# Kernel tuning notes

Measured on AMD Instinct MI355X. Metric: run time of the kernel, lower is better.

Reference implementation:

```python
import jax, jax.numpy as jnp
import numpy as np

L, B, T, S, H, E, V = 2, 128, 64, 80, 512, 512, 32000


def setup_inputs() -> dict:
    key = jax.random.key(0)
    ks = jax.random.split(key, 16)
    s = 1.0 / np.sqrt(H)
    inp = {
        "tokens": jax.random.randint(ks[0], (T, B), 0, V),
        "h0": jax.random.normal(ks[1], (L, B, H), jnp.float32),
        "c0": jax.random.normal(ks[2], (L, B, H), jnp.float32),
        "context": jax.random.normal(ks[3], (B, S, H), jnp.float32),
        "emb_table": jax.random.normal(ks[4], (V, E), jnp.float32) * 0.02,
        # layer 0: input size E+H (input feeding), layer 1: input size H
        "Wih0": jax.random.uniform(ks[5], (4 * H, E + H), jnp.float32, -s, s),
        "Whh0": jax.random.uniform(ks[6], (4 * H, H), jnp.float32, -s, s),
        "bih0": jax.random.uniform(ks[7], (4 * H,), jnp.float32, -s, s),
        "bhh0": jax.random.uniform(ks[8], (4 * H,), jnp.float32, -s, s),
        "Wih1": jax.random.uniform(ks[9], (4 * H, H), jnp.float32, -s, s),
        "Whh1": jax.random.uniform(ks[10], (4 * H, H), jnp.float32, -s, s),
        "bih1": jax.random.uniform(ks[11], (4 * H,), jnp.float32, -s, s),
        "bhh1": jax.random.uniform(ks[12], (4 * H,), jnp.float32, -s, s),
        "W_in": jax.random.uniform(ks[13], (H, H), jnp.float32, -s, s),
        "W_out": jax.random.uniform(ks[14], (H, 2 * H), jnp.float32, -s, s),
    }
    return inp


def _lstm_cell(x, h, c, Wih, Whh, bih, bhh):
    gates = x @ Wih.T + bih + h @ Whh.T + bhh  # [B, 4H]
    i, f, g, o = jnp.split(gates, 4, axis=-1)  # torch LSTMCell gate order
    i, f, o = jax.nn.sigmoid(i), jax.nn.sigmoid(f), jax.nn.sigmoid(o)
    g = jnp.tanh(g)
    c1 = f * c + i * g
    h1 = o * jnp.tanh(c1)
    return h1, c1


def reference(tokens, h0, c0, context, emb_table, Wih0, Whh0, bih0, bhh0,
              Wih1, Whh1, bih1, bhh1, W_in, W_out):
    emb = emb_table[tokens]  # [T, B, E]

    def step(carry, emb_t):
        h, c, out_prev = carry
        x = jnp.concatenate([emb_t, out_prev], axis=1)  # input feeding [B, E+H]
        h0_, c0_ = _lstm_cell(x, h[0], c[0], Wih0, Whh0, bih0, bhh0)
        h1_, c1_ = _lstm_cell(h0_, h[1], c[1], Wih1, Whh1, bih1, bhh1)
        rnn_out = h1_
        # GlobalAttention (Luong general)
        q = rnn_out @ W_in.T                                  # [B, H]
        attn = jax.nn.softmax(jnp.einsum('bsh,bh->bs', context, q), axis=-1)
        wctx = jnp.einsum('bs,bsh->bh', attn, context)        # [B, H]
        out = jnp.tanh(jnp.concatenate([wctx, rnn_out], axis=1) @ W_out.T)
        new_carry = (jnp.stack([h0_, h1_]), jnp.stack([c0_, c1_]), out)
        return new_carry, (out, attn)

    init_out = jnp.zeros((tokens.shape[1], H), emb.dtype)
    (hT, cT, _), (outputs, attns) = jax.lax.scan(step, (h0, c0, init_out), emb)
    return outputs, (hT, cT), attns
```

## Files before the change

kernel.cpp:

```cpp
#include <hip/hip_runtime.h>
#include <hip/hip_fp16.h>
#include <cmath>

typedef _Float16 f16;
typedef _Float16 f16x8 __attribute__((ext_vector_type(8)));
typedef float f32x4 __attribute__((ext_vector_type(4)));
typedef unsigned long long u64;

constexpr int B = 128, T = 64, S = 80, H = 512;
constexpr int BH = B * H;
constexpr int NWG = 512;

#define LB256 __launch_bounds__(256)
#define MFMA16(a, b, c) __builtin_amdgcn_mfma_f32_16x16x32_f16(a, b, c, 0, 0, 0)

__device__ __forceinline__ void astore4(void* p, unsigned v) {
    __hip_atomic_store((unsigned*)p, v, __ATOMIC_RELAXED, __HIP_MEMORY_SCOPE_AGENT);
}
__device__ __forceinline__ void astoref(float* p, float v) {
    __hip_atomic_store(p, v, __ATOMIC_RELAXED, __HIP_MEMORY_SCOPE_AGENT);
}
__device__ __forceinline__ void astore8(void* p, u64 v) {
    __hip_atomic_store((u64*)p, v, __ATOMIC_RELAXED, __HIP_MEMORY_SCOPE_AGENT);
}
__device__ __forceinline__ u64 aload8(const void* p) {
    return __hip_atomic_load((const u64*)p, __ATOMIC_RELAXED, __HIP_MEMORY_SCOPE_AGENT);
}
__device__ __forceinline__ unsigned aload4(const void* p) {
    return __hip_atomic_load((const unsigned*)p, __ATOMIC_RELAXED, __HIP_MEMORY_SCOPE_AGENT);
}

__device__ __forceinline__ void dbar(unsigned* slots, unsigned* go,
                                     unsigned e, int wg) {
    __syncthreads();
    if (threadIdx.x == 0) astore4(&slots[wg * 4], e);
    if (wg == NWG - 1) {
        const int i0 = threadIdx.x * 2;
        while (aload4(&slots[i0 * 4]) < e) __builtin_amdgcn_s_sleep(1);
        while (aload4(&slots[(i0 + 1) * 4]) < e) __builtin_amdgcn_s_sleep(1);
        __syncthreads();
        if (threadIdx.x < 16) astore4(&go[threadIdx.x * 16], e);
    }
    if (threadIdx.x == 0) {
        while (aload4(&go[(wg & 15) * 16]) < e) __builtin_amdgcn_s_sleep(1);
    }
    __syncthreads();
    asm volatile("" ::: "memory");
}

__global__ LB256 void prep_all(
    const float* __restrict__ Wih0, const float* __restrict__ Whh0,
    const float* __restrict__ Wih1, const float* __restrict__ Whh1,
    const float* __restrict__ Wout, const float* __restrict__ Win,
    const float* __restrict__ bih0, const float* __restrict__ bhh0,
    const float* __restrict__ bih1, const float* __restrict__ bhh1,
    const float* __restrict__ h0,
    f16* __restrict__ WB0a, f16* __restrict__ WB0x, f16* __restrict__ WB1p,
    f16* __restrict__ WoutRf, f16* __restrict__ WcatT,
    float* __restrict__ bsum0, float* __restrict__ bsum1,
    f16* __restrict__ h0q, f16* __restrict__ h1q, f16* __restrict__ xq,
    unsigned* __restrict__ slots, unsigned* __restrict__ go)
{
    int stride = gridDim.x * blockDim.x;
    int idx = blockIdx.x * blockDim.x + threadIdx.x;
    for (int i = idx; i < 2048 * 512; i += stride) {
        int rp = i >> 9, k = i & 511;
        int h = rp >> 2, g = rp & 3, src = g * 512 + h;
        WB0a[i] = (f16)Wih0[src * 1024 + k];
    }
    for (int i = idx; i < 2048 * 1024; i += stride) {
        int rp = i >> 10, k = i & 1023;
        int h = rp >> 2, g = rp & 3, src = g * 512 + h;
        float v = (k < 512) ? Wih0[src * 1024 + 512 + k] : Whh0[src * 512 + (k - 512)];
        WB0x[i] = (f16)v;
    }
    for (int i = idx; i < 2048 * 1024; i += stride) {
        int rp = i >> 10, k = i & 1023;
        int h = rp >> 2, g = rp & 3, src = g * 512 + h;
        float v = (k < 512) ? Wih1[src * 512 + k] : Whh1[src * 512 + (k - 512)];
        WB1p[i] = (f16)v;
    }
    for (int i = idx; i < 512 * 512; i += stride) {
        int n = i >> 9, k = i & 511;
        WoutRf[i] = (f16)Wout[n * 1024 + 512 + k];
    }
    for (int i = idx; i < 1024 * 512; i += stride) {
        int r = i >> 9, k = i & 511;
        float v = (r < 512) ? Win[k * 512 + r] : Wout[(r - 512) * 1024 + k];
        WcatT[i] = (f16)v;
    }
    for (int i = idx; i < 2048; i += stride) {
        bsum0[i] = bih0[i] + bhh0[i];
        bsum1[i] = bih1[i] + bhh1[i];
    }
    for (int i = idx; i < BH; i += stride) {
        h0q[i] = (f16)h0[i];
        h1q[i] = (f16)h0[BH + i];
        xq[i] = (f16)0.f;
    }
    for (int i = idx; i < 2048; i += stride) slots[i] = 0u;
    for (int i = idx; i < 256; i += stride) go[i] = 0u;
}

__global__ LB256 void prep_emb(const int* __restrict__ tokens,
                               const float* __restrict__ embtab,
                               f16* __restrict__ embf16)
{
    int stride = gridDim.x * blockDim.x;
    for (int i = blockIdx.x * blockDim.x + threadIdx.x; i < T * B * 512; i += stride) {
        int e = i & 511;
        int tb = i >> 9;
        int tok = tokens[tb];
        embf16[i] = (f16)embtab[(size_t)tok * 512 + e];
    }
}

__global__ LB256 void gemm_ctx(const float* __restrict__ A32,
                               const f16* __restrict__ Wf,
                               f16* __restrict__ Cf)
{
    const int lane = threadIdx.x & 63;
    const int wave = threadIdx.x >> 6;
    const int quad = lane >> 4;
    const int wb = wave >> 1, wn = wave & 1;
    const int m = blockIdx.y * 32 + wb * 16 + (lane & 15);
    const int n = blockIdx.x * 32 + wn * 16 + (lane & 15);

    f32x4 acc = {0.f, 0.f, 0.f, 0.f};
    const float* ar = A32 + (size_t)m * 512;
    const f16* wr = Wf + (size_t)n * 512;
    #pragma unroll 4
    for (int i = 0; i < 16; ++i) {
        int k = i * 32 + quad * 8;
        float4 u0 = *(const float4*)(ar + k);
        float4 u1 = *(const float4*)(ar + k + 4);
        f16x8 av = { (f16)u0.x, (f16)u0.y, (f16)u0.z, (f16)u0.w,
                     (f16)u1.x, (f16)u1.y, (f16)u1.z, (f16)u1.w };
        f16x8 wv = *(const f16x8*)(wr + k);
        acc = MFMA16(av, wv, acc);
    }
    const int col = blockIdx.x * 32 + wn * 16 + (lane & 15);
    #pragma unroll
    for (int r = 0; r < 4; ++r) {
        int row = blockIdx.y * 32 + wb * 16 + quad * 4 + r;
        Cf[(size_t)row * 1024 + col] = (f16)acc[r];
    }
}

__global__ __launch_bounds__(256, 2) void decoder_persist(
    const f16* __restrict__ embf16,
    const f16* __restrict__ WB0a,
    const f16* __restrict__ WB0x,
    const f16* __restrict__ WB1p,
    const f16* __restrict__ WoutRf,
    const f16* __restrict__ ctxWV,
    const float* __restrict__ bsum0, const float* __restrict__ bsum1,
    const float* __restrict__ c0in,
    f16* __restrict__ h0q,
    f16* __restrict__ h1q,
    f16* __restrict__ xq,
    float* __restrict__ scb,
    f16* __restrict__ out2b,
    unsigned* __restrict__ slots, unsigned* __restrict__ go,
    float* __restrict__ out_outputs, float* __restrict__ out_attn,
    float* __restrict__ out_hT, float* __restrict__ out_cT)
{
    const int wg = blockIdx.x, tid = threadIdx.x;
    const int lane = tid & 63, wv_ = tid >> 6, quad = lane >> 4, m16 = lane & 15;
    const int mslice = wg >> 7;
    const int nslice = wg & 127;
    const int b0 = mslice * 32;
    const int rowbase = nslice * 16;

    __shared__ f16 WLA[16 * 1024];
    __shared__ f16 WLB[16 * 1024];
    __shared__ float gbuf[4][32][16];
    __shared__ float scf[80], pp[80];
    __shared__ unsigned o2buf[128];
    __shared__ f16 obuf[256];

    for (int i = tid; i < 2048; i += 256) {
        int r = i >> 7, g = i & 127, gp = g ^ (r & 7);
        *(f16x8*)(WLA + (r * 128 + gp) * 8) =
            *(const f16x8*)(WB0x + ((size_t)(rowbase + r)) * 1024 + g * 8);
        *(f16x8*)(WLB + (r * 128 + gp) * 8) =
            *(const f16x8*)(WB1p + ((size_t)(rowbase + r)) * 1024 + g * 8);
    }
    const int cb_ = b0 + (tid & 31);
    const int jp = (tid >> 5) * 2;
    const int ch = nslice * 4 + jp;
    float c0r[2], c1r[2], bi0[2][4], bi1[2][4];
    if (tid < 64) {
        #pragma unroll
        for (int j = 0; j < 2; ++j) {
            c0r[j] = c0in[cb_ * 512 + ch + j];
            c1r[j] = c0in[BH + cb_ * 512 + ch + j];
            #pragma unroll
            for (int g = 0; g < 4; ++g) {
                bi0[j][g] = bsum0[g * 512 + ch + j];
                bi1[j][g] = bsum1[g * 512 + ch + j];
            }
        }
    }
    const int b_s = wg >> 2;
    const int soff = (wg & 3) * 20;
    const int m2 = wg >> 5, n2 = wg & 31;
    const int b2 = wg >> 1, nh = wg & 1;
    unsigned ep = 0;
    __syncthreads();

    for (int t = 0; t < T; ++t) {
        const f16* EMBt = embf16 + (size_t)t * BH;
        const f16* XPt  = xq  + (size_t)t * BH;
        const f16* H0t  = h0q + (size_t)t * BH;
        const f16* H1t  = h1q + (size_t)t * BH;
        f16* H0n = h0q + (size_t)(t + 1) * BH;
        f16* H1n = h1q + (size_t)(t + 1) * BH;
        f16* XPn = xq  + (size_t)(t + 1) * BH;

        {
            f32x4 ac0 = {0.f, 0.f, 0.f, 0.f}, ac1 = {0.f, 0.f, 0.f, 0.f};
            const int a0r = (b0 + m16) * 512 + quad * 8;
            const int a1r = (b0 + 16 + m16) * 512 + quad * 8;
            const f16* wga = WB0a + (size_t)(rowbase + m16) * 512 + quad * 8;
            const int gq = quad;
            if (wv_ == 0) {
                #pragma unroll
                for (int ks = 0; ks < 12; ++ks) {
                    int k = ks * 32;
                    f16x8 w = *(const f16x8*)(wga + k);
                    ac0 = MFMA16(*(const f16x8*)(EMBt + a0r + k), w, ac0);
                    ac1 = MFMA16(*(const f16x8*)(EMBt + a1r + k), w, ac1);
                }
            } else if (wv_ == 1) {
                #pragma unroll
                for (int ks = 0; ks < 4; ++ks) {
                    int k = 384 + ks * 32;
                    f16x8 w = *(const f16x8*)(wga + k);
                    ac0 = MFMA16(*(const f16x8*)(EMBt + a0r + k), w, ac0);
                    ac1 = MFMA16(*(const f16x8*)(EMBt + a1r + k), w, ac1);
                }
                #pragma unroll
                for (int ks = 0; ks < 8; ++ks) {
                    int k = ks * 32;
                    int gr = (k >> 3) + gq, gp = gr ^ (m16 & 7);
                    f16x8 w = *(const f16x8*)(WLA + (m16 * 128 + gp) * 8);
                    ac0 = MFMA16(*(const f16x8*)(XPt + a0r + k), w, ac0);
                    ac1 = MFMA16(*(const f16x8*)(XPt + a1r + k), w, ac1);
                }
            } else if (wv_ == 2) {
                #pragma unroll
                for (int ks = 0; ks < 8; ++ks) {
                    int k = 256 + ks * 32;
                    int gr = (k >> 3) + gq, gp = gr ^ (m16 & 7);
                    f16x8 w = *(const f16x8*)(WLA + (m16 * 128 + gp) * 8);
                    ac0 = MFMA16(*(const f16x8*)(XPt + a0r + k), w, ac0);
                    ac1 = MFMA16(*(const f16x8*)(XPt + a1r + k), w, ac1);
                }
                #pragma unroll
                for (int ks = 0; ks < 4; ++ks) {
                    int k = ks * 32;
                    int gr = 64 + (k >> 3) + gq, gp = gr ^ (m16 & 7);
                    f16x8 w = *(const f16x8*)(WLA + (m16 * 128 + gp) * 8);
                    ac0 = MFMA16(*(const f16x8*)(H0t + a0r + k), w, ac0);
                    ac1 = MFMA16(*(const f16x8*)(H0t + a1r + k), w, ac1);
                }
            } else {
                #pragma unroll
                for (int ks = 0; ks < 12; ++ks) {
                    int k = 128 + ks * 32;
                    int gr = 64 + (k >> 3) + gq, gp = gr ^ (m16 & 7);
                    f16x8 w = *(const f16x8*)(WLA + (m16 * 128 + gp) * 8);
                    ac0 = MFMA16(*(const f16x8*)(H0t + a0r + k), w, ac0);
                    ac1 = MFMA16(*(const f16x8*)(H0t + a1r + k), w, ac1);
                }
            }
            #pragma unroll
            for (int r = 0; r < 4; ++r) {
                gbuf[wv_][quad * 4 + r][m16] = ac0[r];
                gbuf[wv_][16 + quad * 4 + r][m16] = ac1[r];
            }
            __syncthreads();
            if (tid < 64) {
                const int bl = tid & 31;
                float hv[2];
                #pragma unroll
                for (int j = 0; j < 2; ++j) {
                    int nl = (jp + j) * 4;
                    float z[4];
                    #pragma unroll
                    for (int g = 0; g < 4; ++g)
                        z[g] = gbuf[0][bl][nl + g] + gbuf[1][bl][nl + g] +
                               gbuf[2][bl][nl + g] + gbuf[3][bl][nl + g] + bi0[j][g];
                    float ig = 1.f / (1.f + expf(-z[0]));
                    float fg = 1.f / (1.f + expf(-z[1]));
                    float gg = tanhf(z[2]);
                    float og = 1.f / (1.f + expf(-z[3]));
                    float c = fg * c0r[j] + ig * gg;
                    c0r[j] = c;
                    hv[j] = og * tanhf(c);
                }
                union { f16 f[2]; unsigned u; } pk;
                pk.f[0] = (f16)hv[0]; pk.f[1] = (f16)hv[1];
                astore4(H0n + cb_ * 512 + ch, pk.u);
                if (t == T - 1) {
                    out_hT[cb_ * 512 + ch] = hv[0];
                    out_hT[cb_ * 512 + ch + 1] = hv[1];
                    out_cT[cb_ * 512 + ch] = c0r[0];
                    out_cT[cb_ * 512 + ch + 1] = c0r[1];
                }
            }
        }
        dbar(slots, go, ++ep, wg);

        {
            f32x4 ac0 = {0.f, 0.f, 0.f, 0.f}, ac1 = {0.f, 0.f, 0.f, 0.f};
            const int a0r = (b0 + m16) * 512 + quad * 8;
            const int a1r = (b0 + 16 + m16) * 512 + quad * 8;
            const f16* Asrc = (wv_ < 2) ? H0n : H1t;
            const int k0 = (wv_ & 1) * 256;
            const int gbase = ((wv_ < 2) ? 0 : 64) + (k0 >> 3);
            #pragma unroll
            for (int ks = 0; ks < 8; ++ks) {
                int k = k0 + ks * 32;
                int gr = gbase + ks * 4 + quad, gp = gr ^ (m16 & 7);
                f16x8 w = *(const f16x8*)(WLB + (m16 * 128 + gp) * 8);
                ac0 = MFMA16(*(const f16x8*)(Asrc + a0r + k), w, ac0);
                ac1 = MFMA16(*(const f16x8*)(Asrc + a1r + k), w, ac1);
            }
            #pragma unroll
            for (int r = 0; r < 4; ++r) {
                gbuf[wv_][quad * 4 + r][m16] = ac0[r];
                gbuf[wv_][16 + quad * 4 + r][m16] = ac1[r];
            }
            __syncthreads();
            if (tid < 64) {
                const int bl = tid & 31;
                float hv[2];
                #pragma unroll
                for (int j = 0; j < 2; ++j) {
                    int nl = (jp + j) * 4;
                    float z[4];
                    #pragma unroll
                    for (int g = 0; g < 4; ++g)
                        z[g] = gbuf[0][bl][nl + g] + gbuf[1][bl][nl + g] +
                               gbuf[2][bl][nl + g] + gbuf[3][bl][nl + g] + bi1[j][g];
                    float ig = 1.f / (1.f + expf(-z[0]));
                    float fg = 1.f / (1.f + expf(-z[1]));
                    float gg = tanhf(z[2]);
                    float og = 1.f / (1.f + expf(-z[3]));
                    float c = fg * c1r[j] + ig * gg;
                    c1r[j] = c;
                    hv[j] = og * tanhf(c);
                }
                union { f16 f[2]; unsigned u; } pk;
                pk.f[0] = (f16)hv[0]; pk.f[1] = (f16)hv[1];
                astore4(H1n + cb_ * 512 + ch, pk.u);
                if (t == T - 1) {
                    out_hT[BH + cb_ * 512 + ch] = hv[0];
                    out_hT[BH + cb_ * 512 + ch + 1] = hv[1];
                    out_cT[BH + cb_ * 512 + ch] = c1r[0];
                    out_cT[BH + cb_ * 512 + ch + 1] = c1r[1];
                }
            }
        }
        dbar(slots, go, ++ep, wg);

        {
            const f16* hrow = H1n + b_s * 512;
            f16x8 hfrag = *(const f16x8*)(hrow + lane * 8);
            #pragma unroll
            for (int i = 0; i < 5; ++i) {
                int s = soff + wv_ * 5 + i;
                const f16* cr = ctxWV + ((size_t)(b_s * 80 + s)) * 1024 + lane * 8;
                f16x8 a = *(const f16x8*)cr;
                float d = 0.f;
                #pragma unroll
                for (int j = 0; j < 8; ++j) d += (float)a[j] * (float)hfrag[j];
                #pragma unroll
                for (int o = 32; o > 0; o >>= 1) d += __shfl_xor(d, o);
                if (lane == 0) astoref(&scb[b_s * 80 + s], d);
            }
            if (wg < 128) {
                f32x4 ac0 = {0.f, 0.f, 0.f, 0.f}, ac1 = {0.f, 0.f, 0.f, 0.f};
                const int bb0 = m2 * 32;
                const int a0r = (bb0 + m16) * 512 + quad * 8;
                const int a1r = (bb0 + 16 + m16) * 512 + quad * 8;
                const f16* wr = WoutRf + (size_t)(n2 * 16 + m16) * 512 + quad * 8;
                const int k0 = wv_ * 128;
                #pragma unroll
                for (int ks = 0; ks < 4; ++ks) {
                    int k = k0 + ks * 32;
                    f16x8 w = *(const f16x8*)(wr + k);
                    ac0 = MFMA16(*(const f16x8*)(H1n + a0r + k), w, ac0);
                    ac1 = MFMA16(*(const f16x8*)(H1n + a1r + k), w, ac1);
                }
                __syncthreads();
                #pragma unroll
                for (int r = 0; r < 4; ++r) {
                    gbuf[wv_][quad * 4 + r][m16] = ac0[r];
                    gbuf[wv_][16 + quad * 4 + r][m16] = ac1[r];
                }
                __syncthreads();
                const int bl = tid >> 3, np = (tid & 7) * 2;
                float v0 = gbuf[0][bl][np] + gbuf[1][bl][np] + gbuf[2][bl][np] + gbuf[3][bl][np];
                float v1 = gbuf[0][bl][np+1] + gbuf[1][bl][np+1] + gbuf[2][bl][np+1] + gbuf[3][bl][np+1];
                union { f16 f[2]; unsigned u; } pk;
                pk.f[0] = (f16)v0; pk.f[1] = (f16)v1;
                astore4(out2b + (bb0 + bl) * 512 + n2 * 16 + np, pk.u);
            }
        }
        dbar(slots, go, ++ep, wg);

        if (wg < 256) {
            if (wv_ == 0 && lane < 40) {
                union { u64 u; float f[2]; } v;
                v.u = aload8(&scb[b2 * 80 + lane * 2]);
                scf[lane * 2] = v.f[0];
                scf[lane * 2 + 1] = v.f[1];
            }
            if (tid < 128)
                o2buf[tid] = aload4((const unsigned*)(out2b + b2 * 512 + nh * 256) + tid);
            __syncthreads();
            if (wv_ == 0) {
                float e0 = scf[lane];
                float e1 = (lane < 16) ? scf[64 + lane] : -1e30f;
                float m = fmaxf(e0, e1);
                #pragma unroll
                for (int o = 32; o > 0; o >>= 1) m = fmaxf(m, __shfl_xor(m, o));
                float x0 = expf(e0 - m);
                float x1 = (lane < 16) ? expf(e1 - m) : 0.f;
                float su = x0 + x1;
                #pragma unroll
                for (int o = 32; o > 0; o >>= 1) su += __shfl_xor(su, o);
                float inv = 1.f / su;
                float p0 = x0 * inv;
                pp[lane] = p0;
                if (nh == 0) out_attn[((size_t)t * 128 + b2) * 80 + lane] = p0;
                if (lane < 16) {
                    float p1 = x1 * inv;
                    pp[64 + lane] = p1;
                    if (nh == 0) out_attn[((size_t)t * 128 + b2) * 80 + 64 + lane] = p1;
                }
            }
            __syncthreads();
            const int n = nh * 256 + tid;
            float acc = 0.f;
            const f16* cv = ctxWV + (size_t)b2 * 80 * 1024 + 512 + n;
            #pragma unroll 8
            for (int s = 0; s < 80; ++s) acc += pp[s] * (float)cv[(size_t)s * 1024];
            float o2 = (float)((const f16*)o2buf)[tid];
            float o = tanhf(acc + o2);
            out_outputs[(size_t)t * BH + b2 * 512 + n] = o;
            obuf[tid] = (f16)o;
            __syncthreads();
            if (tid < 64)
                astore8(XPn + b2 * 512 + nh * 256 + tid * 4, ((const u64*)obuf)[tid]);
        }
        dbar(slots, go, ++ep, wg);
    }
}

extern "C" void kernel_launch(void* const* d_in, const int* in_sizes, int n_in,
                              void* d_out, int out_size, void* d_ws, size_t ws_size,
                              hipStream_t stream)
{
    const int*   tokens  = (const int*)  d_in[0];
    const float* h0      = (const float*)d_in[1];
    const float* c0      = (const float*)d_in[2];
    const float* context = (const float*)d_in[3];
    const float* embtab  = (const float*)d_in[4];
    const float* Wih0    = (const float*)d_in[5];
    const float* Whh0    = (const float*)d_in[6];
    const float* bih0    = (const float*)d_in[7];
    const float* bhh0    = (const float*)d_in[8];
    const float* Wih1    = (const float*)d_in[9];
    const float* Whh1    = (const float*)d_in[10];
    const float* bih1    = (const float*)d_in[11];
    const float* bhh1    = (const float*)d_in[12];
    const float* Win     = (const float*)d_in[13];
    const float* Wout    = (const float*)d_in[14];

    float* outF        = (float*)d_out;
    float* out_outputs = outF;
    float* out_hT      = outF + (size_t)T * BH;
    float* out_cT      = out_hT + 2 * BH;
    float* out_attn    = out_cT + 2 * BH;

    char* w = (char*)d_ws;
    auto alloc = [&](size_t bytes) {
        char* p = w;
        w += (bytes + 255) & ~(size_t)255;
        return p;
    };
    f16*      WB0a   = (f16*)     alloc((size_t)2048 * 512 * 2);
    f16*      WB0x   = (f16*)     alloc((size_t)2048 * 1024 * 2);
    f16*      WB1p   = (f16*)     alloc((size_t)2048 * 1024 * 2);
    f16*      WoutRf = (f16*)     alloc((size_t)512 * 512 * 2);
    f16*      WcatT  = (f16*)     alloc((size_t)1024 * 512 * 2);
    f16*      embf16 = (f16*)     alloc((size_t)T * B * 512 * 2);
    f16*      ctxWV  = (f16*)     alloc((size_t)B * S * 1024 * 2);
    float*    bsum0  = (float*)   alloc(2048 * 4);
    float*    bsum1  = (float*)   alloc(2048 * 4);
    f16*      h0q    = (f16*)     alloc((size_t)(T + 1) * BH * 2);
    f16*      h1q    = (f16*)     alloc((size_t)(T + 1) * BH * 2);
    f16*      xq     = (f16*)     alloc((size_t)(T + 1) * BH * 2);
    float*    scb    = (float*)   alloc((size_t)B * 80 * 4);
    f16*      out2b  = (f16*)     alloc((size_t)B * 512 * 2);
    unsigned* slots  = (unsigned*)alloc(2048 * 4);
    unsigned* go     = (unsigned*)alloc(256 * 4);

    prep_all<<<1024, 256, 0, stream>>>(Wih0, Whh0, Wih1, Whh1, Wout, Win,
                                       bih0, bhh0, bih1, bhh1, h0,
                                       WB0a, WB0x, WB1p, WoutRf, WcatT,
                                       bsum0, bsum1, h0q, h1q, xq, slots, go);
    prep_emb<<<2048, 256, 0, stream>>>(tokens, embtab, embf16);
    gemm_ctx<<<dim3(32, 320), 256, 0, stream>>>(context, WcatT, ctxWV);

    decoder_persist<<<NWG, 256, 0, stream>>>(
        embf16, WB0a, WB0x, WB1p, WoutRf, ctxWV, bsum0, bsum1, c0,
        h0q, h1q, xq, scb, out2b, slots, go,
        out_outputs, out_attn, out_hT, out_cT);
}
```

Baseline: 2.078 ms.

## Replace grid-wide barriers with per-batch-slice barriers and fuse attention output stage

Swaps the global two-level barrier for a barrier that waits only on the 128 workgroups sharing the same batch slice. It also remaps workgroup indices so slices interleave. The attention score, softmax and output projection now run inside one phase per batch row. Each group computes its own scores and the Wout·h1 dot products redundantly, which removes one grid barrier and the scratch buffers per step. The cost is redundant score computation (4x per batch row) and scalar Wout dot products in place of MFMA.

```diff
diff --git a/kernel.cpp b/kernel.cpp
--- a/kernel.cpp
+++ b/kernel.cpp
@@ -17,32 +17,20 @@
 __device__ __forceinline__ void astore4(void* p, unsigned v) {
     __hip_atomic_store((unsigned*)p, v, __ATOMIC_RELAXED, __HIP_MEMORY_SCOPE_AGENT);
 }
-__device__ __forceinline__ void astoref(float* p, float v) {
-    __hip_atomic_store(p, v, __ATOMIC_RELAXED, __HIP_MEMORY_SCOPE_AGENT);
-}
 __device__ __forceinline__ void astore8(void* p, u64 v) {
     __hip_atomic_store((u64*)p, v, __ATOMIC_RELAXED, __HIP_MEMORY_SCOPE_AGENT);
 }
-__device__ __forceinline__ u64 aload8(const void* p) {
-    return __hip_atomic_load((const u64*)p, __ATOMIC_RELAXED, __HIP_MEMORY_SCOPE_AGENT);
-}
 __device__ __forceinline__ unsigned aload4(const void* p) {
     return __hip_atomic_load((const unsigned*)p, __ATOMIC_RELAXED, __HIP_MEMORY_SCOPE_AGENT);
 }
 
-__device__ __forceinline__ void dbar(unsigned* slots, unsigned* go,
-                                     unsigned e, int wg) {
+__device__ __forceinline__ void mbar(unsigned* slots, unsigned e,
+                                     int mslice, int nslice) {
     __syncthreads();
-    if (threadIdx.x == 0) astore4(&slots[wg * 4], e);
-    if (wg == NWG - 1) {
-        const int i0 = threadIdx.x * 2;
-        while (aload4(&slots[i0 * 4]) < e) __builtin_amdgcn_s_sleep(1);
-        while (aload4(&slots[(i0 + 1) * 4]) < e) __builtin_amdgcn_s_sleep(1);
-        __syncthreads();
-        if (threadIdx.x < 16) astore4(&go[threadIdx.x * 16], e);
-    }
-    if (threadIdx.x == 0) {
-        while (aload4(&go[(wg & 15) * 16]) < e) __builtin_amdgcn_s_sleep(1);
+    if (threadIdx.x == 0) astore4(&slots[(mslice * 128 + nslice) * 4], e);
+    if (threadIdx.x < 128) {
+        while (aload4(&slots[(mslice * 128 + threadIdx.x) * 4]) < e)
+            __builtin_amdgcn_s_sleep(1);
     }
     __syncthreads();
     asm volatile("" ::: "memory");
@@ -59,7 +47,7 @@
     f16* __restrict__ WoutRf, f16* __restrict__ WcatT,
     float* __restrict__ bsum0, float* __restrict__ bsum1,
     f16* __restrict__ h0q, f16* __restrict__ h1q, f16* __restrict__ xq,
-    unsigned* __restrict__ slots, unsigned* __restrict__ go)
+    unsigned* __restrict__ slots)
 {
     int stride = gridDim.x * blockDim.x;
     int idx = blockIdx.x * blockDim.x + threadIdx.x;
@@ -99,7 +87,6 @@
         xq[i] = (f16)0.f;
     }
     for (int i = idx; i < 2048; i += stride) slots[i] = 0u;
-    for (int i = idx; i < 256; i += stride) go[i] = 0u;
 }
 
 __global__ LB256 void prep_emb(const int* __restrict__ tokens,
@@ -159,16 +146,14 @@
     f16* __restrict__ h0q,
     f16* __restrict__ h1q,
     f16* __restrict__ xq,
-    float* __restrict__ scb,
-    f16* __restrict__ out2b,
-    unsigned* __restrict__ slots, unsigned* __restrict__ go,
+    unsigned* __restrict__ slots,
     float* __restrict__ out_outputs, float* __restrict__ out_attn,
     float* __restrict__ out_hT, float* __restrict__ out_cT)
 {
     const int wg = blockIdx.x, tid = threadIdx.x;
     const int lane = tid & 63, wv_ = tid >> 6, quad = lane >> 4, m16 = lane & 15;
-    const int mslice = wg >> 7;
-    const int nslice = wg & 127;
+    const int mslice = (wg & 7) >> 1;
+    const int nslice = ((wg >> 3) << 1) | (wg & 1);
     const int b0 = mslice * 32;
     const int rowbase = nslice * 16;
 
@@ -176,8 +161,9 @@
     __shared__ f16 WLB[16 * 1024];
     __shared__ float gbuf[4][32][16];
     __shared__ float scf[80], pp[80];
-    __shared__ unsigned o2buf[128];
-    __shared__ f16 obuf[256];
+    __shared__ float psum[2][128];
+    __shared__ __align__(8) f16 h1s[512];
+    __shared__ __align__(8) f16 obuf[128];
 
     for (int i = tid; i < 2048; i += 256) {
         int r = i >> 7, g = i & 127, gp = g ^ (r & 7);
@@ -202,10 +188,9 @@
             }
         }
     }
-    const int b_s = wg >> 2;
-    const int soff = (wg & 3) * 20;
-    const int m2 = wg >> 5, n2 = wg & 31;
-    const int b2 = wg >> 1, nh = wg & 1;
+    const int q = nslice & 3;
+    const int bloc = nslice >> 2;
+    const int cb2 = b0 + bloc;
     unsigned ep = 0;
     __syncthreads();
 
@@ -311,7 +296,7 @@
                 }
             }
         }
-        dbar(slots, go, ++ep, wg);
+        mbar(slots, ++ep, mslice, nslice);
 
         {
             f32x4 ac0 = {0.f, 0.f, 0.f, 0.f}, ac1 = {0.f, 0.f, 0.f, 0.f};
@@ -364,63 +349,25 @@
                 }
             }
         }
-        dbar(slots, go, ++ep, wg);
+        mbar(slots, ++ep, mslice, nslice);
 
         {
-            const f16* hrow = H1n + b_s * 512;
-            f16x8 hfrag = *(const f16x8*)(hrow + lane * 8);
-            #pragma unroll
-            for (int i = 0; i < 5; ++i) {
-                int s = soff + wv_ * 5 + i;
-                const f16* cr = ctxWV + ((size_t)(b_s * 80 + s)) * 1024 + lane * 8;
+            if (tid < 128)
+                ((u64*)h1s)[tid] = ((const u64*)(H1n + cb2 * 512))[tid];
+            __syncthreads();
+            f16x8 hfrag = *(const f16x8*)&h1s[lane * 8];
+            #pragma unroll 4
+            for (int i = 0; i < 20; ++i) {
+                int s = wv_ * 20 + i;
+                const f16* cr = ctxWV + ((size_t)(cb2 * 80 + s)) * 1024 + lane * 8;
                 f16x8 a = *(const f16x8*)cr;
                 float d = 0.f;
                 #pragma unroll
                 for (int j = 0; j < 8; ++j) d += (float)a[j] * (float)hfrag[j];
                 #pragma unroll
                 for (int o = 32; o > 0; o >>= 1) d += __shfl_xor(d, o);
-                if (lane == 0) astoref(&scb[b_s * 80 + s], d);
-            }
-            if (wg < 128) {
-                f32x4 ac0 = {0.f, 0.f, 0.f, 0.f}, ac1 = {0.f, 0.f, 0.f, 0.f};
-                const int bb0 = m2 * 32;
-                const int a0r = (bb0 + m16) * 512 + quad * 8;
-                const int a1r = (bb0 + 16 + m16) * 512 + quad * 8;
-                const f16* wr = WoutRf + (size_t)(n2 * 16 + m16) * 512 + quad * 8;
-                const int k0 = wv_ * 128;
-                #pragma unroll
-                for (int ks = 0; ks < 4; ++ks) {
-                    int k = k0 + ks * 32;
-                    f16x8 w = *(const f16x8*)(wr + k);
-                    ac0 = MFMA16(*(const f16x8*)(H1n + a0r + k), w, ac0);
-                    ac1 = MFMA16(*(const f16x8*)(H1n + a1r + k), w, ac1);
-                }
-                __syncthreads();
-                #pragma unroll
-                for (int r = 0; r < 4; ++r) {
-                    gbuf[wv_][quad * 4 + r][m16] = ac0[r];
-                    gbuf[wv_][16 + quad * 4 + r][m16] = ac1[r];
-                }
-                __syncthreads();
-                const int bl = tid >> 3, np = (tid & 7) * 2;
-                float v0 = gbuf[0][bl][np] + gbuf[1][bl][np] + gbuf[2][bl][np] + gbuf[3][bl][np];
-                float v1 = gbuf[0][bl][np+1] + gbuf[1][bl][np+1] + gbuf[2][bl][np+1] + gbuf[3][bl][np+1];
-                union { f16 f[2]; unsigned u; } pk;
-                pk.f[0] = (f16)v0; pk.f[1] = (f16)v1;
-                astore4(out2b + (bb0 + bl) * 512 + n2 * 16 + np, pk.u);
-            }
-        }
-        dbar(slots, go, ++ep, wg);
-
-        if (wg < 256) {
-            if (wv_ == 0 && lane < 40) {
-                union { u64 u; float f[2]; } v;
-                v.u = aload8(&scb[b2 * 80 + lane * 2]);
-                scf[lane * 2] = v.f[0];
-                scf[lane * 2 + 1] = v.f[1];
-            }
-            if (tid < 128)
-                o2buf[tid] = aload4((const unsigned*)(out2b + b2 * 512 + nh * 256) + tid);
+                if (lane == 0) scf[s] = d;
+            }
             __syncthreads();
             if (wv_ == 0) {
                 float e0 = scf[lane];
@@ -436,28 +383,51 @@
                 float inv = 1.f / su;
                 float p0 = x0 * inv;
                 pp[lane] = p0;
-                if (nh == 0) out_attn[((size_t)t * 128 + b2) * 80 + lane] = p0;
+                if (q == 0) out_attn[((size_t)t * 128 + cb2) * 80 + lane] = p0;
                 if (lane < 16) {
                     float p1 = x1 * inv;
                     pp[64 + lane] = p1;
-                    if (nh == 0) out_attn[((size_t)t * 128 + b2) * 80 + 64 + lane] = p1;
-                }
-            }
-            __syncthreads();
-            const int n = nh * 256 + tid;
+                    if (q == 0) out_attn[((size_t)t * 128 + cb2) * 80 + 64 + lane] = p1;
+                }
+            }
+            __syncthreads();
+            const int nl = tid & 127, kh = tid >> 7;
+            const int n = q * 128 + nl;
             float acc = 0.f;
-            const f16* cv = ctxWV + (size_t)b2 * 80 * 1024 + 512 + n;
-            #pragma unroll 8
-            for (int s = 0; s < 80; ++s) acc += pp[s] * (float)cv[(size_t)s * 1024];
-            float o2 = (float)((const f16*)o2buf)[tid];
-            float o = tanhf(acc + o2);
-            out_outputs[(size_t)t * BH + b2 * 512 + n] = o;
-            obuf[tid] = (f16)o;
-            __syncthreads();
-            if (tid < 64)
-                astore8(XPn + b2 * 512 + nh * 256 + tid * 4, ((const u64*)obuf)[tid]);
+            if (kh == 0) {
+                const f16* cv = ctxWV + (size_t)cb2 * 80 * 1024 + 512 + n;
+                #pragma unroll 8
+                for (int s = 0; s < 80; ++s) acc += pp[s] * (float)cv[(size_t)s * 1024];
+                const f16* wr = WoutRf + (size_t)n * 512;
+                #pragma unroll
+                for (int kk = 0; kk < 24; ++kk) {
+                    f16x8 w = *(const f16x8*)(wr + kk * 8);
+                    f16x8 h = *(const f16x8*)&h1s[kk * 8];
+                    #pragma unroll
+                    for (int j = 0; j < 8; ++j) acc += (float)w[j] * (float)h[j];
+                }
+            } else {
+                const f16* wr = WoutRf + (size_t)n * 512;
+                #pragma unroll
+                for (int kk = 24; kk < 64; ++kk) {
+                    f16x8 w = *(const f16x8*)(wr + kk * 8);
+                    f16x8 h = *(const f16x8*)&h1s[kk * 8];
+                    #pragma unroll
+                    for (int j = 0; j < 8; ++j) acc += (float)w[j] * (float)h[j];
+                }
+            }
+            psum[kh][nl] = acc;
+            __syncthreads();
+            if (tid < 128) {
+                float o = tanhf(psum[0][tid] + psum[1][tid]);
+                out_outputs[(size_t)t * BH + cb2 * 512 + n] = o;
+                obuf[tid] = (f16)o;
+            }
+            __syncthreads();
+            if (tid < 32)
+                astore8(XPn + cb2 * 512 + q * 128 + tid * 4, ((const u64*)obuf)[tid]);
         }
-        dbar(slots, go, ++ep, wg);
+        mbar(slots, ++ep, mslice, nslice);
     }
 }
 
@@ -505,20 +475,17 @@
     f16*      h0q    = (f16*)     alloc((size_t)(T + 1) * BH * 2);
     f16*      h1q    = (f16*)     alloc((size_t)(T + 1) * BH * 2);
     f16*      xq     = (f16*)     alloc((size_t)(T + 1) * BH * 2);
-    float*    scb    = (float*)   alloc((size_t)B * 80 * 4);
-    f16*      out2b  = (f16*)     alloc((size_t)B * 512 * 2);
     unsigned* slots  = (unsigned*)alloc(2048 * 4);
-    unsigned* go     = (unsigned*)alloc(256 * 4);
 
     prep_all<<<1024, 256, 0, stream>>>(Wih0, Whh0, Wih1, Whh1, Wout, Win,
                                        bih0, bhh0, bih1, bhh1, h0,
                                        WB0a, WB0x, WB1p, WoutRf, WcatT,
-                                       bsum0, bsum1, h0q, h1q, xq, slots, go);
+                                       bsum0, bsum1, h0q, h1q, xq, slots);
     prep_emb<<<2048, 256, 0, stream>>>(tokens, embtab, embf16);
     gemm_ctx<<<dim3(32, 320), 256, 0, stream>>>(context, WcatT, ctxWV);
 
     decoder_persist<<<NWG, 256, 0, stream>>>(
         embf16, WB0a, WB0x, WB1p, WoutRf, ctxWV, bsum0, bsum1, c0,
-        h0q, h1q, xq, scb, out2b, slots, go,
+        h0q, h1q, xq, slots,
         out_outputs, out_attn, out_hT, out_cT);
 }
```

New measurement: 3.165 ms. 1.52x slower.

## Remap workgroup-to-batch assignment so attention phases stay within an XCD

Applied to the files above, without the earlier changes.

Workgroup roles are re-indexed by wg&7 (likely the XCD id under round-robin dispatch), so each XCD owns a 16-batch slice for the score, W_out projection and softmax phases. The projection tile changes from 32 batch rows by 16 columns to 16 rows by 32 columns, sharing one A fragment across two MFMAs. The aim is to keep the data passed between phases within one XCD's L2 and to cut cross-die traffic, at the cost of relying on an assumed dispatch order and of changing which workgroups do the softmax work.

```diff
diff --git a/kernel.cpp b/kernel.cpp
--- a/kernel.cpp
+++ b/kernel.cpp
@@ -202,10 +202,12 @@
             }
         }
     }
-    const int b_s = wg >> 2;
-    const int soff = (wg & 3) * 20;
-    const int m2 = wg >> 5, n2 = wg & 31;
-    const int b2 = wg >> 1, nh = wg & 1;
+    const int xid = wg & 7;
+    const int xr = wg >> 3;
+    const int b_s = xid * 16 + (xr & 15);
+    const int soff = (xr >> 4) * 20;
+    const int b2 = xid * 16 + ((xr - 16) >> 1);
+    const int nh = (xr - 16) & 1;
     unsigned ep = 0;
     __syncthreads();
 
@@ -381,19 +383,18 @@
                 for (int o = 32; o > 0; o >>= 1) d += __shfl_xor(d, o);
                 if (lane == 0) astoref(&scb[b_s * 80 + s], d);
             }
-            if (wg < 128) {
+            if (xr < 16) {
                 f32x4 ac0 = {0.f, 0.f, 0.f, 0.f}, ac1 = {0.f, 0.f, 0.f, 0.f};
-                const int bb0 = m2 * 32;
-                const int a0r = (bb0 + m16) * 512 + quad * 8;
-                const int a1r = (bb0 + 16 + m16) * 512 + quad * 8;
-                const f16* wr = WoutRf + (size_t)(n2 * 16 + m16) * 512 + quad * 8;
+                const int arow = (xid * 16 + m16) * 512 + quad * 8;
+                const f16* wr0 = WoutRf + (size_t)(xr * 32 + m16) * 512 + quad * 8;
+                const f16* wr1 = WoutRf + (size_t)(xr * 32 + 16 + m16) * 512 + quad * 8;
                 const int k0 = wv_ * 128;
                 #pragma unroll
                 for (int ks = 0; ks < 4; ++ks) {
                     int k = k0 + ks * 32;
-                    f16x8 w = *(const f16x8*)(wr + k);
-                    ac0 = MFMA16(*(const f16x8*)(H1n + a0r + k), w, ac0);
-                    ac1 = MFMA16(*(const f16x8*)(H1n + a1r + k), w, ac1);
+                    f16x8 a = *(const f16x8*)(H1n + arow + k);
+                    ac0 = MFMA16(a, *(const f16x8*)(wr0 + k), ac0);
+                    ac1 = MFMA16(a, *(const f16x8*)(wr1 + k), ac1);
                 }
                 __syncthreads();
                 #pragma unroll
@@ -402,17 +403,21 @@
                     gbuf[wv_][16 + quad * 4 + r][m16] = ac1[r];
                 }
                 __syncthreads();
-                const int bl = tid >> 3, np = (tid & 7) * 2;
-                float v0 = gbuf[0][bl][np] + gbuf[1][bl][np] + gbuf[2][bl][np] + gbuf[3][bl][np];
-                float v1 = gbuf[0][bl][np+1] + gbuf[1][bl][np+1] + gbuf[2][bl][np+1] + gbuf[3][bl][np+1];
+                const int tile = tid >> 7, bl = (tid >> 3) & 15, np = (tid & 7) * 2;
+                const int grow = tile * 16 + bl;
+                const int gr0 = tile * 16 + ((tid >> 3) & 15);
+                (void)grow;
+                float v0 = gbuf[0][gr0][np] + gbuf[1][gr0][np] + gbuf[2][gr0][np] + gbuf[3][gr0][np];
+                float v1 = gbuf[0][gr0][np+1] + gbuf[1][gr0][np+1] + gbuf[2][gr0][np+1] + gbuf[3][gr0][np+1];
                 union { f16 f[2]; unsigned u; } pk;
                 pk.f[0] = (f16)v0; pk.f[1] = (f16)v1;
-                astore4(out2b + (bb0 + bl) * 512 + n2 * 16 + np, pk.u);
+                const int n = xr * 32 + tile * 16 + np;
+                astore4(out2b + (xid * 16 + bl) * 512 + n, pk.u);
             }
         }
         dbar(slots, go, ++ep, wg);
 
-        if (wg < 256) {
+        if (xr >= 16 && xr < 48) {
             if (wv_ == 0 && lane < 40) {
                 union { u64 u; float f[2]; } v;
                 v.u = aload8(&scb[b2 * 80 + lane * 2]);
```

Result: faster. 2.036 ms (-2.0%).
